# Kernel tuning notes

Measured on AMD Instinct MI355X. Metric: run time of the kernel, lower is better.

## Reference

```python
import jax, jax.numpy as jnp
import numpy as np

C = 64  # chunk size (hardcoded in DeltaCorrection.forward)


def setup_inputs() -> dict:
    key = jax.random.key(0)
    ks = jax.random.split(key, 6)
    B, H, N, d = 4, 16, 4096, 64
    q = jax.random.normal(ks[0], (B, H, N, d), jnp.float32)
    k = jax.random.normal(ks[1], (B, H, N, d), jnp.float32)
    v = jax.random.normal(ks[2], (B, H, N, d), jnp.float32)
    # gate projections: Linear(d, 1). Use small random weights so gates vary per token.
    w_decay = jax.random.normal(ks[3], (d, 1), jnp.float32) * 0.1
    b_decay = jnp.full((1,), -2.0, jnp.float32)
    w_write = jax.random.normal(ks[4], (d, 1), jnp.float32) * 0.1
    b_write = jnp.full((1,), -1.0, jnp.float32)
    out_scale = jnp.full((1,), 0.01, jnp.float32)
    return {"q": q, "k": k, "v": v, "w_decay": w_decay, "b_decay": b_decay,
            "w_write": w_write, "b_write": b_write, "out_scale": out_scale}


def _delta_correction(q, k, v, w_decay, b_decay, w_write, b_write, out_scale):
    B, H, N, d = q.shape
    assert N % C == 0  # pad branch is a no-op for our shapes
    beta = jax.nn.sigmoid(k @ w_write + b_write)   # (B,H,N,1) write strength
    alpha = jax.nn.sigmoid(k @ w_decay + b_decay)  # (B,H,N,1) decay
    k_norm = k / jnp.maximum(jnp.linalg.norm(k, axis=-1, keepdims=True), 1e-12)

    n_chunks = N // C
    q_c = q.reshape(B, H, n_chunks, C, d)
    k_c = k_norm.reshape(B, H, n_chunks, C, d)
    v_c = v.reshape(B, H, n_chunks, C, d)
    b_c = beta.reshape(B, H, n_chunks, C, 1)
    a_c = alpha.reshape(B, H, n_chunks, C, 1)

    # intra-chunk causal linear attention, scaled by per-key beta
    scores = jnp.einsum('bhnid,bhnjd->bhnij', q_c, k_c)      # (B,H,n,C,C)
    causal = jnp.tril(jnp.ones((C, C), q.dtype))
    scores = scores * causal * jnp.swapaxes(b_c, -1, -2)
    intra = jnp.einsum('bhnij,bhnjd->bhnid', scores, v_c)     # (B,H,n,C,d)

    # inter-chunk: sequential (d,d) state propagation via scan
    chunk_decay = jnp.mean(a_c, axis=3) ** C                  # (B,H,n,1)
    kv_all = jnp.einsum('bhnci,bhncj->bhnij', b_c * v_c, k_c) # (B,H,n,d,d)

    def step(S, inp):
        qc, kvc, dec = inp  # (B,H,C,d), (B,H,d,d), (B,H,1)
        inter = jnp.einsum('bhij,bhcj->bhci', S, qc)
        S = dec[..., None] * S + kvc
        return S, inter

    xs = (jnp.moveaxis(q_c, 2, 0), jnp.moveaxis(kv_all, 2, 0),
          jnp.moveaxis(chunk_decay, 2, 0))
    S0 = jnp.zeros((B, H, d, d), q.dtype)
    _, inter = jax.lax.scan(step, S0, xs)                     # (n,B,H,C,d)
    inter = jnp.moveaxis(inter, 0, 2)                         # (B,H,n,C,d)

    corrections = (intra + inter).reshape(B, H, N, d)
    return corrections * out_scale[0]


def reference(q, k, v, w_decay, b_decay, w_write, b_write, out_scale):
    return _delta_correction(q, k, v, w_decay, b_decay, w_write, b_write, out_scale)
```

## Files before the change

kernel.cpp:

```cpp
#include <hip/hip_runtime.h>
#include <math.h>


#define NCH 64
#define NBH 64

typedef __attribute__((ext_vector_type(8))) short bf16x8;
typedef __attribute__((ext_vector_type(4))) float f32x4;
typedef unsigned short ushort_t;

#define MFMA(a, b, c) __builtin_amdgcn_mfma_f32_16x16x32_bf16(a, b, c, 0, 0, 0)
#define GETC(v, u) ((u) == 0 ? (v).x : ((u) == 1 ? (v).y : ((u) == 2 ? (v).z : (v).w)))

__device__ __forceinline__ float sigf(float x) { return 1.0f / (1.0f + expf(-x)); }

__device__ __forceinline__ int swb(int row, int col) {
  return ((row << 7) + (col << 1)) ^ ((row & 7) << 4);
}

__device__ __forceinline__ void split1(float x, ushort_t& h, ushort_t& l) {
  unsigned xb = __float_as_uint(x);
  h = (ushort_t)(xb >> 16);
  float hf = __uint_as_float(xb & 0xFFFF0000u);
  float lf = x - hf;
  l = (ushort_t)(__float_as_uint(lf) >> 16);
}

__device__ __forceinline__ void st_split4(char* bh, char* bl, int row, int col, float4 v) {
  ushort_t h0, h1, h2, h3, l0, l1, l2, l3;
  split1(v.x, h0, l0); split1(v.y, h1, l1); split1(v.z, h2, l2); split1(v.w, h3, l3);
  uint2 hp, lp;
  hp.x = (unsigned)h0 | ((unsigned)h1 << 16); hp.y = (unsigned)h2 | ((unsigned)h3 << 16);
  lp.x = (unsigned)l0 | ((unsigned)l1 << 16); lp.y = (unsigned)l2 | ((unsigned)l3 << 16);
  int o = swb(row, col);
  *(uint2*)(bh + o) = hp;
  *(uint2*)(bl + o) = lp;
}

__device__ __forceinline__ bf16x8 ldfrag(const char* base, int mrow, int kk, int lane) {
  int r = mrow + (lane & 15);
  int c = kk + ((lane >> 4) << 3);
  return *(const bf16x8*)(base + swb(r, c));
}

__device__ __forceinline__ void split8(float4 a, float4 b, bf16x8& h, bf16x8& l) {
  float x[8] = {a.x, a.y, a.z, a.w, b.x, b.y, b.z, b.w};
  bf16x8 hh, ll;
#pragma unroll
  for (int i = 0; i < 8; ++i) {
    ushort_t hi, lo;
    split1(x[i], hi, lo);
    hh[i] = (short)hi; ll[i] = (short)lo;
  }
  h = hh; l = ll;
}

__global__ __launch_bounds__(256, 4) void k1_kvdecay(
    const float* __restrict__ kg, const float* __restrict__ vg,
    const float* __restrict__ w_decay, const float* __restrict__ b_decay,
    const float* __restrict__ w_write, const float* __restrict__ b_write,
    float* __restrict__ ws_kv, float* __restrict__ ws_decay) {
  __shared__ uint4 smraw[2064];
  char* sm = (char*)smraw;
  char* KT_H = sm;
  char* KT_L = sm + 8192;
  char* VT_H = sm + 16384;
  char* VT_L = sm + 24576;
  float* abuf = (float*)(sm + 32768);

  const int tid = threadIdx.x;
  const int lane = tid & 63, wv = tid >> 6;
  const int bh = blockIdx.x >> 6, cid = blockIdx.x & 63;
  const size_t gbase = (size_t)(bh * 4096 + cid * 64) * 64;

  {
    const int t = tid >> 2, g = tid & 3;
    const float* kp = kg + gbase + t * 64 + g * 16;
    const float* vp = vg + gbase + t * 64 + g * 16;
    float4 kr[4], vr[4];
#pragma unroll
    for (int u = 0; u < 4; ++u) { kr[u] = *(const float4*)(kp + 4 * u); vr[u] = *(const float4*)(vp + 4 * u); }
    float n2 = 0.f, dw = 0.f, da = 0.f;
#pragma unroll
    for (int u = 0; u < 4; ++u) {
      const float* wwp = w_write + g * 16 + 4 * u;
      const float* wdp = w_decay + g * 16 + 4 * u;
      float4 k4 = kr[u];
      n2 = fmaf(k4.x, k4.x, fmaf(k4.y, k4.y, fmaf(k4.z, k4.z, fmaf(k4.w, k4.w, n2))));
      dw = fmaf(k4.x, wwp[0], fmaf(k4.y, wwp[1], fmaf(k4.z, wwp[2], fmaf(k4.w, wwp[3], dw))));
      da = fmaf(k4.x, wdp[0], fmaf(k4.y, wdp[1], fmaf(k4.z, wdp[2], fmaf(k4.w, wdp[3], da))));
    }
    n2 += __shfl_xor(n2, 1, 64); n2 += __shfl_xor(n2, 2, 64);
    dw += __shfl_xor(dw, 1, 64); dw += __shfl_xor(dw, 2, 64);
    da += __shfl_xor(da, 1, 64); da += __shfl_xor(da, 2, 64);
    float beta  = sigf(dw + b_write[0]);
    float alpha = sigf(da + b_decay[0]);
    float fold  = beta / fmaxf(sqrtf(n2), 1e-12f);
    if (g == 0) abuf[t] = alpha;
#pragma unroll
    for (int u = 0; u < 4; ++u) {
      float kf[4] = {kr[u].x * fold, kr[u].y * fold, kr[u].z * fold, kr[u].w * fold};
      float vf[4] = {vr[u].x, vr[u].y, vr[u].z, vr[u].w};
#pragma unroll
      for (int e = 0; e < 4; ++e) {
        int row = g * 16 + 4 * u + e;
        ushort_t h, l;
        int o = swb(row, t);
        split1(kf[e], h, l);
        *(ushort_t*)(KT_H + o) = h; *(ushort_t*)(KT_L + o) = l;
        split1(vf[e], h, l);
        *(ushort_t*)(VT_H + o) = h; *(ushort_t*)(VT_L + o) = l;
      }
    }
  }
  __syncthreads();

  if (tid < 64) {
    float a = abuf[tid];
    for (int off = 32; off; off >>= 1) a += __shfl_down(a, off, 64);
    if (tid == 0) {
      float m = a * (1.0f / 64.0f);
      float p = m * m; p = p * p; p = p * p; p = p * p; p = p * p; p = p * p;
      ws_decay[bh * NCH + cid] = p;
    }
  }

  f32x4 z = {0.f, 0.f, 0.f, 0.f};
  f32x4 acc[4] = {z, z, z, z};
#pragma unroll
  for (int kk = 0; kk < 64; kk += 32) {
    bf16x8 ah = ldfrag(VT_H, wv * 16, kk, lane);
    bf16x8 al = ldfrag(VT_L, wv * 16, kk, lane);
#pragma unroll
    for (int jb = 0; jb < 4; ++jb) {
      bf16x8 bh_ = ldfrag(KT_H, jb * 16, kk, lane);
      bf16x8 bl_ = ldfrag(KT_L, jb * 16, kk, lane);
      acc[jb] = MFMA(ah, bh_, acc[jb]);
      acc[jb] = MFMA(ah, bl_, acc[jb]);
      acc[jb] = MFMA(al, bh_, acc[jb]);
    }
  }
  float* kvout = ws_kv + (size_t)(bh * NCH + cid) * 4096;
  {
    int i0 = wv * 16 + ((lane >> 4) << 2);
#pragma unroll
    for (int jb = 0; jb < 4; ++jb) {
      int j = jb * 16 + (lane & 15);
#pragma unroll
      for (int r = 0; r < 4; ++r) kvout[(i0 + r) * 64 + j] = acc[jb][r];
    }
  }
}

__global__ __launch_bounds__(256) void k2_scan(float* __restrict__ ws_kv,
                                               const float* __restrict__ ws_decay) {
  const int bh = blockIdx.x >> 2;
  const int pos = (blockIdx.x & 3) * 256 + threadIdx.x;
  float4* base = (float4*)ws_kv + (size_t)bh * 65536 + pos;
  const float* dec = ws_decay + bh * NCH;
  float4 S = make_float4(0.f, 0.f, 0.f, 0.f);
#pragma unroll
  for (int gq = 0; gq < 8; ++gq) {
    float4 buf[8];
#pragma unroll
    for (int j = 0; j < 8; ++j) buf[j] = base[(size_t)(gq * 8 + j) * 1024];
#pragma unroll
    for (int j = 0; j < 8; ++j) {
      int c = gq * 8 + j;
      float dcy = dec[c];
      base[(size_t)c * 1024] = S;
      S.x = fmaf(dcy, S.x, buf[j].x);
      S.y = fmaf(dcy, S.y, buf[j].y);
      S.z = fmaf(dcy, S.z, buf[j].z);
      S.w = fmaf(dcy, S.w, buf[j].w);
    }
  }
}

__global__ __launch_bounds__(256, 3) void k3_out(
    const float* __restrict__ qg, const float* __restrict__ kg,
    const float* __restrict__ vg,
    const float* __restrict__ w_write, const float* __restrict__ b_write,
    const float* __restrict__ out_scale,
    const float* __restrict__ ws_kv, float* __restrict__ outg) {
  __shared__ uint4 smraw[3072];
  char* sm = (char*)smraw;
  char* QS_H = sm;             char* QS_L = sm + 8192;
  char* KS_H = sm + 16384;     char* KS_L = sm + 24576;
  char* VT_H = sm + 32768;     char* VT_L = sm + 40960;
  char* PS_H = KS_H;           char* PS_L = KS_L;

  const int tid = threadIdx.x;
  const int lane = tid & 63, wv = tid >> 6;
  const int bh = blockIdx.x >> 6, cid = blockIdx.x & 63;
  const size_t gbase = (size_t)(bh * 4096 + cid * 64) * 64;
  const float* Sg = ws_kv + (size_t)(bh * NCH + cid) * 4096;

#pragma unroll
  for (int rr = 0; rr < 4; ++rr) {
    int f = tid + 256 * rr;
    int row = f >> 4, c4 = (f & 15) * 4;
    float4 qq = *(const float4*)(qg + gbase + row * 64 + c4);
    st_split4(QS_H, QS_L, row, c4, qq);
  }
  {
    const int rq = tid & 15, cq = tid >> 4;
    float4 vv[4];
#pragma unroll
    for (int e = 0; e < 4; ++e)
      vv[e] = *(const float4*)(vg + gbase + (4 * rq + e) * 64 + 4 * cq);
#pragma unroll
    for (int m = 0; m < 4; ++m) {
      float4 tv = make_float4(GETC(vv[0], m), GETC(vv[1], m), GETC(vv[2], m), GETC(vv[3], m));
      st_split4(VT_H, VT_L, 4 * cq + m, 4 * rq, tv);
    }
  }
  {
    const int t = tid >> 2, g = tid & 3;
    const float* kp = kg + gbase + t * 64 + g * 16;
    float4 kr[4];
#pragma unroll
    for (int u = 0; u < 4; ++u) kr[u] = *(const float4*)(kp + 4 * u);
    float n2 = 0.f, dw = 0.f;
#pragma unroll
    for (int u = 0; u < 4; ++u) {
      const float* wwp = w_write + g * 16 + 4 * u;
      float4 k4 = kr[u];
      n2 = fmaf(k4.x, k4.x, fmaf(k4.y, k4.y, fmaf(k4.z, k4.z, fmaf(k4.w, k4.w, n2))));
      dw = fmaf(k4.x, wwp[0], fmaf(k4.y, wwp[1], fmaf(k4.z, wwp[2], fmaf(k4.w, wwp[3], dw))));
    }
    n2 += __shfl_xor(n2, 1, 64); n2 += __shfl_xor(n2, 2, 64);
    dw += __shfl_xor(dw, 1, 64); dw += __shfl_xor(dw, 2, 64);
    float beta = sigf(dw + b_write[0]);
    float fold = beta / fmaxf(sqrtf(n2), 1e-12f);
#pragma unroll
    for (int u = 0; u < 4; ++u) {
      float4 kf4 = make_float4(kr[u].x * fold, kr[u].y * fold, kr[u].z * fold, kr[u].w * fold);
      st_split4(KS_H, KS_L, t, g * 16 + 4 * u, kf4);
    }
  }
  __syncthreads();

  f32x4 z = {0.f, 0.f, 0.f, 0.f};
  f32x4 accs[4] = {z, z, z, z};
#pragma unroll
  for (int kk = 0; kk < 64; kk += 32) {
    bf16x8 ah = ldfrag(KS_H, wv * 16, kk, lane);
    bf16x8 al = ldfrag(KS_L, wv * 16, kk, lane);
#pragma unroll
    for (int nb = 0; nb < 4; ++nb) {
      bf16x8 bh_ = ldfrag(QS_H, nb * 16, kk, lane);
      bf16x8 bl_ = ldfrag(QS_L, nb * 16, kk, lane);
      accs[nb] = MFMA(ah, bh_, accs[nb]);
      accs[nb] = MFMA(ah, bl_, accs[nb]);
      accs[nb] = MFMA(al, bh_, accs[nb]);
    }
  }
  __syncthreads();

  float4 sraw[16];
  {
    const int l15 = lane & 15, g8 = (lane >> 4) << 3;
#pragma unroll
    for (int ib = 0; ib < 4; ++ib) {
#pragma unroll
      for (int k2 = 0; k2 < 2; ++k2) {
        const float* p = Sg + (ib * 16 + l15) * 64 + k2 * 32 + g8;
        sraw[ib * 4 + k2 * 2 + 0] = *(const float4*)(p);
        sraw[ib * 4 + k2 * 2 + 1] = *(const float4*)(p + 4);
      }
    }
  }

#pragma unroll
  for (int nb = 0; nb < 4; ++nb) {
    int tcol = nb * 16 + (lane & 15);
    int j0 = wv * 16 + ((lane >> 4) << 2);
    float x0 = (j0 + 0 <= tcol) ? accs[nb][0] : 0.f;
    float x1 = (j0 + 1 <= tcol) ? accs[nb][1] : 0.f;
    float x2 = (j0 + 2 <= tcol) ? accs[nb][2] : 0.f;
    float x3 = (j0 + 3 <= tcol) ? accs[nb][3] : 0.f;
    st_split4(PS_H, PS_L, tcol, j0, make_float4(x0, x1, x2, x3));
  }
  __syncthreads();

  f32x4 acco[4] = {z, z, z, z};
#pragma unroll
  for (int k2 = 0; k2 < 2; ++k2) {
    const int kk = k2 * 32;
    bf16x8 qh = ldfrag(QS_H, wv * 16, kk, lane);
    bf16x8 ql = ldfrag(QS_L, wv * 16, kk, lane);
    bf16x8 ph = ldfrag(PS_H, wv * 16, kk, lane);
    bf16x8 pl = ldfrag(PS_L, wv * 16, kk, lane);
#pragma unroll
    for (int ib = 0; ib < 4; ++ib) {
      bf16x8 sh, sl;
      split8(sraw[ib * 4 + k2 * 2 + 0], sraw[ib * 4 + k2 * 2 + 1], sh, sl);
      acco[ib] = MFMA(qh, sh, acco[ib]);
      acco[ib] = MFMA(qh, sl, acco[ib]);
      acco[ib] = MFMA(ql, sh, acco[ib]);
      bf16x8 vh = ldfrag(VT_H, ib * 16, kk, lane);
      bf16x8 vl = ldfrag(VT_L, ib * 16, kk, lane);
      acco[ib] = MFMA(ph, vh, acco[ib]);
      acco[ib] = MFMA(ph, vl, acco[ib]);
      acco[ib] = MFMA(pl, vh, acco[ib]);
    }
  }

  const float osc = out_scale[0];
  {
    int t0 = wv * 16 + ((lane >> 4) << 2);
    int l15 = lane & 15;
#pragma unroll
    for (int ib = 0; ib < 4; ++ib) {
#pragma unroll
      for (int r = 0; r < 4; ++r)
        outg[gbase + (t0 + r) * 64 + ib * 16 + l15] = acco[ib][r] * osc;
    }
  }
}

extern "C" void kernel_launch(void* const* d_in, const int* in_sizes, int n_in,
                              void* d_out, int out_size, void* d_ws, size_t ws_size,
                              hipStream_t stream) {
  const float* q         = (const float*)d_in[0];
  const float* k         = (const float*)d_in[1];
  const float* v         = (const float*)d_in[2];
  const float* w_decay   = (const float*)d_in[3];
  const float* b_decay   = (const float*)d_in[4];
  const float* w_write   = (const float*)d_in[5];
  const float* b_write   = (const float*)d_in[6];
  const float* out_scale = (const float*)d_in[7];
  float* out = (float*)d_out;

  float* ws_kv    = (float*)d_ws;
  float* ws_decay = ws_kv + (size_t)NBH * NCH * 4096;

  k1_kvdecay<<<dim3(NBH * NCH), dim3(256), 0, stream>>>(
      k, v, w_decay, b_decay, w_write, b_write, ws_kv, ws_decay);
  k2_scan<<<dim3(256), dim3(256), 0, stream>>>(ws_kv, ws_decay);
  k3_out<<<dim3(NBH * NCH), dim3(256), 0, stream>>>(
      q, k, v, w_write, b_write, out_scale, ws_kv, out);
}
```

Measured before the change: 288.7 us.

## Pre-split scan state into bf16 hi/lo, skip masked score tiles, prefetch state

```diff
diff --git a/kernel.cpp b/kernel.cpp
--- a/kernel.cpp
+++ b/kernel.cpp
@@ -41,18 +41,6 @@
   int r = mrow + (lane & 15);
   int c = kk + ((lane >> 4) << 3);
   return *(const bf16x8*)(base + swb(r, c));
-}
-
-__device__ __forceinline__ void split8(float4 a, float4 b, bf16x8& h, bf16x8& l) {
-  float x[8] = {a.x, a.y, a.z, a.w, b.x, b.y, b.z, b.w};
-  bf16x8 hh, ll;
-#pragma unroll
-  for (int i = 0; i < 8; ++i) {
-    ushort_t hi, lo;
-    split1(x[i], hi, lo);
-    hh[i] = (short)hi; ll[i] = (short)lo;
-  }
-  h = hh; l = ll;
 }
 
 __global__ __launch_bounds__(256, 4) void k1_kvdecay(
@@ -156,23 +144,29 @@
                                                const float* __restrict__ ws_decay) {
   const int bh = blockIdx.x >> 2;
   const int pos = (blockIdx.x & 3) * 256 + threadIdx.x;
-  float4* base = (float4*)ws_kv + (size_t)bh * 65536 + pos;
+  uint4* base = (uint4*)ws_kv + (size_t)bh * 65536 + pos;
   const float* dec = ws_decay + bh * NCH;
   float4 S = make_float4(0.f, 0.f, 0.f, 0.f);
 #pragma unroll
   for (int gq = 0; gq < 8; ++gq) {
-    float4 buf[8];
-#pragma unroll
-    for (int j = 0; j < 8; ++j) buf[j] = base[(size_t)(gq * 8 + j) * 1024];
+    uint4 raw[8];
+#pragma unroll
+    for (int j = 0; j < 8; ++j) raw[j] = base[(size_t)(gq * 8 + j) * 1024];
 #pragma unroll
     for (int j = 0; j < 8; ++j) {
       int c = gq * 8 + j;
       float dcy = dec[c];
-      base[(size_t)c * 1024] = S;
-      S.x = fmaf(dcy, S.x, buf[j].x);
-      S.y = fmaf(dcy, S.y, buf[j].y);
-      S.z = fmaf(dcy, S.z, buf[j].z);
-      S.w = fmaf(dcy, S.w, buf[j].w);
+      float4 kv = *(float4*)&raw[j];
+      ushort_t h0, h1, h2, h3, l0, l1, l2, l3;
+      split1(S.x, h0, l0); split1(S.y, h1, l1); split1(S.z, h2, l2); split1(S.w, h3, l3);
+      uint4 w;
+      w.x = (unsigned)h0 | ((unsigned)h1 << 16); w.y = (unsigned)h2 | ((unsigned)h3 << 16);
+      w.z = (unsigned)l0 | ((unsigned)l1 << 16); w.w = (unsigned)l2 | ((unsigned)l3 << 16);
+      base[(size_t)c * 1024] = w;
+      S.x = fmaf(dcy, S.x, kv.x);
+      S.y = fmaf(dcy, S.y, kv.y);
+      S.z = fmaf(dcy, S.z, kv.z);
+      S.w = fmaf(dcy, S.w, kv.w);
     }
   }
 }
@@ -194,7 +188,21 @@
   const int lane = tid & 63, wv = tid >> 6;
   const int bh = blockIdx.x >> 6, cid = blockIdx.x & 63;
   const size_t gbase = (size_t)(bh * 4096 + cid * 64) * 64;
-  const float* Sg = ws_kv + (size_t)(bh * NCH + cid) * 4096;
+
+  uint4 scell[16];
+  {
+    const uint4* Sg4 = (const uint4*)(ws_kv) + (size_t)(bh * NCH + cid) * 1024;
+    const int l15 = lane & 15, cc0 = (lane >> 4) << 1;
+#pragma unroll
+    for (int ib = 0; ib < 4; ++ib) {
+#pragma unroll
+      for (int k2 = 0; k2 < 2; ++k2) {
+        const uint4* p = Sg4 + (ib * 16 + l15) * 16 + k2 * 8 + cc0;
+        scell[ib * 4 + k2 * 2 + 0] = p[0];
+        scell[ib * 4 + k2 * 2 + 1] = p[1];
+      }
+    }
+  }
 
 #pragma unroll
   for (int rr = 0; rr < 4; ++rr) {
@@ -241,47 +249,47 @@
   }
   __syncthreads();
 
-  f32x4 z = {0.f, 0.f, 0.f, 0.f};
-  f32x4 accs[4] = {z, z, z, z};
-#pragma unroll
-  for (int kk = 0; kk < 64; kk += 32) {
-    bf16x8 ah = ldfrag(KS_H, wv * 16, kk, lane);
-    bf16x8 al = ldfrag(KS_L, wv * 16, kk, lane);
-#pragma unroll
-    for (int nb = 0; nb < 4; ++nb) {
-      bf16x8 bh_ = ldfrag(QS_H, nb * 16, kk, lane);
-      bf16x8 bl_ = ldfrag(QS_L, nb * 16, kk, lane);
-      accs[nb] = MFMA(ah, bh_, accs[nb]);
-      accs[nb] = MFMA(ah, bl_, accs[nb]);
-      accs[nb] = MFMA(al, bh_, accs[nb]);
-    }
-  }
+  const f32x4 z = {0.f, 0.f, 0.f, 0.f};
+  f32x4 sc0 = z, sc1 = z, sc2 = z;
+  auto tileA = [&](int jb, int tb, f32x4& acc) {
+#pragma unroll
+    for (int kk = 0; kk < 64; kk += 32) {
+      bf16x8 ah = ldfrag(KS_H, jb * 16, kk, lane);
+      bf16x8 al = ldfrag(KS_L, jb * 16, kk, lane);
+      bf16x8 bh_ = ldfrag(QS_H, tb * 16, kk, lane);
+      bf16x8 bl_ = ldfrag(QS_L, tb * 16, kk, lane);
+      acc = MFMA(ah, bh_, acc);
+      acc = MFMA(ah, bl_, acc);
+      acc = MFMA(al, bh_, acc);
+    }
+  };
+  if (wv == 0)      { tileA(0, 0, sc0); tileA(1, 1, sc1); tileA(2, 2, sc2); }
+  else if (wv == 1) { tileA(3, 3, sc0); tileA(0, 1, sc1); tileA(1, 2, sc2); }
+  else if (wv == 2) { tileA(2, 3, sc0); tileA(0, 2, sc1); }
+  else              { tileA(1, 3, sc0); tileA(0, 3, sc1); }
   __syncthreads();
 
-  float4 sraw[16];
-  {
-    const int l15 = lane & 15, g8 = (lane >> 4) << 3;
-#pragma unroll
-    for (int ib = 0; ib < 4; ++ib) {
-#pragma unroll
-      for (int k2 = 0; k2 < 2; ++k2) {
-        const float* p = Sg + (ib * 16 + l15) * 64 + k2 * 32 + g8;
-        sraw[ib * 4 + k2 * 2 + 0] = *(const float4*)(p);
-        sraw[ib * 4 + k2 * 2 + 1] = *(const float4*)(p + 4);
-      }
-    }
-  }
-
-#pragma unroll
-  for (int nb = 0; nb < 4; ++nb) {
-    int tcol = nb * 16 + (lane & 15);
-    int j0 = wv * 16 + ((lane >> 4) << 2);
-    float x0 = (j0 + 0 <= tcol) ? accs[nb][0] : 0.f;
-    float x1 = (j0 + 1 <= tcol) ? accs[nb][1] : 0.f;
-    float x2 = (j0 + 2 <= tcol) ? accs[nb][2] : 0.f;
-    float x3 = (j0 + 3 <= tcol) ? accs[nb][3] : 0.f;
+  auto psMask = [&](int jb, int tb, f32x4 a) {
+    int tcol = tb * 16 + (lane & 15);
+    int j0 = jb * 16 + ((lane >> 4) << 2);
+    float x0 = (j0 + 0 <= tcol) ? a[0] : 0.f;
+    float x1 = (j0 + 1 <= tcol) ? a[1] : 0.f;
+    float x2 = (j0 + 2 <= tcol) ? a[2] : 0.f;
+    float x3 = (j0 + 3 <= tcol) ? a[3] : 0.f;
     st_split4(PS_H, PS_L, tcol, j0, make_float4(x0, x1, x2, x3));
-  }
+  };
+  auto psFull = [&](int jb, int tb, f32x4 a) {
+    st_split4(PS_H, PS_L, tb * 16 + (lane & 15), jb * 16 + ((lane >> 4) << 2),
+              make_float4(a[0], a[1], a[2], a[3]));
+  };
+  auto psZero = [&](int jb, int tb) {
+    st_split4(PS_H, PS_L, tb * 16 + (lane & 15), jb * 16 + ((lane >> 4) << 2),
+              make_float4(0.f, 0.f, 0.f, 0.f));
+  };
+  if (wv == 0)      { psMask(0, 0, sc0); psMask(1, 1, sc1); psMask(2, 2, sc2); psZero(1, 0); psZero(2, 1); }
+  else if (wv == 1) { psMask(3, 3, sc0); psFull(0, 1, sc1); psFull(1, 2, sc2); psZero(2, 0); psZero(3, 2); }
+  else if (wv == 2) { psFull(2, 3, sc0); psFull(0, 2, sc1); psZero(3, 0); }
+  else              { psFull(1, 3, sc0); psFull(0, 3, sc1); psZero(3, 1); }
   __syncthreads();
 
   f32x4 acco[4] = {z, z, z, z};
@@ -294,8 +302,12 @@
     bf16x8 pl = ldfrag(PS_L, wv * 16, kk, lane);
 #pragma unroll
     for (int ib = 0; ib < 4; ++ib) {
-      bf16x8 sh, sl;
-      split8(sraw[ib * 4 + k2 * 2 + 0], sraw[ib * 4 + k2 * 2 + 1], sh, sl);
+      uint4 cA = scell[ib * 4 + k2 * 2 + 0];
+      uint4 cB = scell[ib * 4 + k2 * 2 + 1];
+      uint4 th = make_uint4(cA.x, cA.y, cB.x, cB.y);
+      uint4 tl = make_uint4(cA.z, cA.w, cB.z, cB.w);
+      bf16x8 sh = *(bf16x8*)&th;
+      bf16x8 sl = *(bf16x8*)&tl;
       acco[ib] = MFMA(qh, sh, acco[ib]);
       acco[ib] = MFMA(qh, sl, acco[ib]);
       acco[ib] = MFMA(ql, sh, acco[ib]);
```

Measured after the change: 283.5 us. No clear change (-1.8%).
